# Kernel tuning notes

Measured on AMD Instinct MI355X. Metric: run time of the kernel, lower is better.

## Reference

```python
import jax, jax.numpy as jnp
import numpy as np

B, N, K = 64, 1024, 20
HEADS, DIM_K, DIM_V, CH_RAISE = 8, 32, 32, 64
C_CAT = 4 * 2 + DIM_V  # 44


def setup_inputs() -> dict:
    key = jax.random.key(0)
    ks = jax.random.split(key, 16)

    def w(k, shape):
        fan_in = shape[-1]
        return jax.random.normal(k, shape, dtype=jnp.float32) / np.sqrt(fan_in)

    def gamma(k, n):
        return 1.0 + 0.1 * jax.random.normal(k, (n,), dtype=jnp.float32)

    def beta(k, n):
        return 0.1 * jax.random.normal(k, (n,), dtype=jnp.float32)

    return {
        "x": jax.random.normal(ks[0], (B, N, 4), dtype=jnp.float32),
        "W_h": w(ks[1], (DIM_V, 4)),              # mlp_h: conv2d 4 -> dim_v, 1x1
        "W1": w(ks[2], (CH_RAISE, C_CAT)),        # mlp conv2d 44 -> 64
        "g1": gamma(ks[3], CH_RAISE), "b1": beta(ks[4], CH_RAISE),
        "W2": w(ks[5], (CH_RAISE, CH_RAISE)),     # mlp conv2d 64 -> 64
        "g2": gamma(ks[6], CH_RAISE), "b2": beta(ks[7], CH_RAISE),
        "W_v": w(ks[8], (DIM_V, C_CAT)),          # mlp_v conv1d 44 -> 32
        "gv": gamma(ks[9], DIM_V), "bv": beta(ks[10], DIM_V),
        "W_k": w(ks[11], (DIM_K, C_CAT)),         # mlp_k conv1d 44 -> 32
        "W_q": w(ks[12], (HEADS * DIM_K, CH_RAISE)),  # mlp_q conv1d 64 -> 256
        "gq": gamma(ks[13], HEADS * DIM_K), "bq": beta(ks[14], HEADS * DIM_K),
    }


def _forward(x, W_h, W1, g1, b1, W2, g2, b2, W_v, gv, bv, W_k, W_q, gq, bq):
    xyz = x[..., :4]                 # [B,N,4]
    feat = xyz                       # use_norm=False -> feature = xyz
    b, n, _ = xyz.shape

    # squared pairwise distances [B,N,N]
    sq = jnp.sum(xyz * xyz, axis=-1)
    dist = -2.0 * jnp.einsum('bnc,bmc->bnm', xyz, xyz) + sq[:, :, None] + sq[:, None, :]

    # KNN: K smallest distances
    _, knn_idx = jax.lax.top_k(-dist, K)          # [B,N,K]
    bidx = jnp.arange(b)[:, None, None]
    neighbor_xyz = xyz[bidx, knn_idx]             # [B,N,K,4]
    grouped = feat[bidx, knn_idx]                 # [B,N,K,4]

    feat_t = jnp.transpose(feat, (0, 2, 1))       # [B,4,N]
    grouped_c = jnp.transpose(grouped, (0, 3, 1, 2))          # [B,4,N,K]
    gnorm = grouped_c - feat_t[..., None]                     # [B,4,N,K]
    rel = jnp.transpose(neighbor_xyz - xyz[:, :, None, :], (0, 3, 1, 2))  # [B,4,N,K]

    pos = jnp.einsum('vc,bcnk->bvnk', W_h, rel)               # [B,32,N,K]
    center = jnp.broadcast_to(feat_t[..., None], (b, 4, n, K))
    feature = jnp.concatenate([gnorm, center, pos], axis=1)   # [B,44,N,K]

    # mlp: two 1x1 conv + BN(eval, affine) + ReLU
    h = jnp.einsum('oc,bcnk->bonk', W1, feature)
    h = jax.nn.relu(g1[None, :, None, None] * h + b1[None, :, None, None])
    h = jnp.einsum('oc,bcnk->bonk', W2, h)
    h = jax.nn.relu(g2[None, :, None, None] * h + b2[None, :, None, None])
    feature_q = jnp.max(h, axis=-1)                           # [B,64,N]

    q = jnp.einsum('oc,bcn->bon', W_q, feature_q)             # [B,256,N]
    q = jax.nn.relu(gq[None, :, None] * q + bq[None, :, None])
    q = q.reshape(b, HEADS, DIM_K, n)                         # [B,h,d,N]

    v = jnp.einsum('vc,bcnk->bvnk', W_v, feature)             # [B,32,N,K]
    v = gv[None, :, None, None] * v + bv[None, :, None, None]
    v = jnp.transpose(v, (0, 2, 1, 3))                        # [B,N,v,K]

    kk = jnp.einsum('dc,bcnk->bdnk', W_k, feature)            # [B,32,N,K]
    kk = jax.nn.softmax(kk, axis=-1)
    kk = jnp.transpose(kk, (0, 2, 1, 3))                      # [B,N,d,K]

    kv = jnp.einsum('bndk,bnvk->bdvn', kk, v)                 # [B,d,v,N]
    out = jnp.einsum('bhdn,bdvn->bhvn', q, kv)                # [B,h,v,N]
    out = out.reshape(b, HEADS * DIM_V, n)                    # [B,256,N]
    return xyz, out


def reference(x, W_h, W1, g1, b1, W2, g2, b2, W_v, gv, bv, W_k, W_q, gq, bq):
    return _forward(x, W_h, W1, g1, b1, W2, g2, b2, W_v, gv, bv, W_k, W_q, gq, bq)
```

## Files before the change

### kernel.cpp

```cpp
#include <hip/hip_runtime.h>
#include <math.h>

#define NPTS 1024
#define KNBR 20
#define CH 64


typedef __attribute__((ext_vector_type(8))) short s16x8;
typedef __attribute__((ext_vector_type(4))) float f32x4;

static __device__ __forceinline__ ushort f2bf(float f) {
  uint u = __float_as_uint(f);
  uint r = (u + 0x7FFFu + ((u >> 16) & 1u)) >> 16;
  return (ushort)r;
}

static __device__ __forceinline__ uint pkbf(float a, float b) {
  uint ua = __float_as_uint(a) + 0x8000u;
  uint ub = __float_as_uint(b) + 0x8000u;
  return __builtin_amdgcn_perm(ub, ua, 0x07060302);
}

static __device__ __forceinline__ int mbcnt64(unsigned long long m) {
  return __builtin_amdgcn_mbcnt_hi((uint)(m >> 32),
                                   __builtin_amdgcn_mbcnt_lo((uint)m, 0));
}

__global__ __launch_bounds__(256) void k_prep(
    const float* __restrict__ Wh, const float* __restrict__ W1,
    const float* __restrict__ g1, const float* __restrict__ b1,
    const float* __restrict__ Wv, const float* __restrict__ Wk,
    const float* __restrict__ W2, const float* __restrict__ Wq,
    float* __restrict__ wp, ushort* __restrict__ w2b,
    ushort* __restrict__ wqb, ushort* __restrict__ w1b) {
  int t = threadIdx.x;
  {
    int o = t >> 2, c = t & 3;
    float acc = W1[o * 40 + c];
    #pragma unroll
    for (int v = 0; v < 32; ++v) acc = fmaf(W1[o * 40 + 8 + v], Wh[v * 4 + c], acc);
    float g = g1[o];
    wp[t] = g * acc;
    wp[256 + t] = g * W1[o * 40 + 4 + c];
  }
  if (t < 128) {
    int d = t >> 2, c = t & 3;
    float av = Wv[d * 40 + c];
    float ak = Wk[d * 40 + c];
    #pragma unroll
    for (int u = 0; u < 32; ++u) {
      av = fmaf(Wv[d * 40 + 8 + u], Wh[u * 4 + c], av);
      ak = fmaf(Wk[d * 40 + 8 + u], Wh[u * 4 + c], ak);
    }
    wp[512 + t] = av;
    wp[640 + t] = Wv[d * 40 + 4 + c];
    wp[768 + t] = ak;
    wp[896 + t] = Wk[d * 40 + 4 + c];
  }
  #pragma unroll
  for (int i = 0; i < 16; ++i) w2b[t * 16 + i] = f2bf(W2[t * 16 + i]);
  for (int i = 0; i < 64; ++i) wqb[t * 64 + i] = f2bf(Wq[t * 64 + i]);
  __syncthreads();
  for (int idx = t; idx < 2048; idx += 256) {
    int ch = idx >> 5, kk = idx & 31;
    float v = 0.f;
    if (kk < 4) v = wp[ch * 4 + kk];
    else if (kk < 8) v = wp[256 + ch * 4 + (kk - 4)];
    else if (kk == 8) v = b1[ch];
    w1b[idx] = f2bf(v);
  }
}

__global__ __launch_bounds__(256) void k_knn(const float4* __restrict__ xv,
                                             ushort* __restrict__ knn,
                                             float4* __restrict__ outx) {
  __shared__ float4 sx[NPTS];
  __shared__ float ssq[NPTS];
  __shared__ uint s_sk[4][64];
  __shared__ ushort s_sj[4][64];

  int t = threadIdx.x;
  int b = blockIdx.x >> 5, grp = blockIdx.x & 31;
  for (int j = t; j < NPTS; j += 256) {
    float4 p = xv[b * NPTS + j];
    sx[j] = p;
    ssq[j] = p.x * p.x + p.y * p.y + p.z * p.z + p.w * p.w;
    if (grp == 0) outx[b * NPTS + j] = p;
  }
  __syncthreads();

  int w = t >> 6, l = t & 63;

  #pragma unroll 1
  for (int i = 0; i < 8; ++i) {
    int cloc = grp * 32 + w * 8 + i;
    int gid20 = (b * NPTS + cloc) * KNBR;
    float4 c = sx[cloc];
    uint u[16];
    uint mn = 0xFFFFFFFFu;
    #pragma unroll
    for (int s = 0; s < 16; ++s) {
      int j = s * 64 + l;
      float4 q = sx[j];
      float dot = c.x * q.x;
      dot = fmaf(c.y, q.y, dot);
      dot = fmaf(c.z, q.z, dot);
      dot = fmaf(c.w, q.w, dot);
      float key = fmaf(-2.f, dot, ssq[j]);
      uint uu = __float_as_uint(key);
      uu = ((int)uu < 0) ? ~uu : (uu | 0x80000000u);
      u[s] = uu;
      mn = min(mn, uu);
    }

    uint T0 = 0;
    #pragma unroll
    for (int bit = 31; bit >= 0; --bit) {
      uint cand = T0 | (1u << bit);
      if (__popcll(__ballot(mn < cand)) < 20) T0 = cand;
    }

    int scnt = 0;
    #pragma unroll
    for (int s = 0; s < 16; ++s) scnt += (int)__popcll(__ballot(u[s] <= T0));

    if (scnt <= 64) {
      int base = 0;
      #pragma unroll
      for (int s = 0; s < 16; ++s) {
        unsigned long long mask = __ballot(u[s] <= T0);
        if (u[s] <= T0) {
          int off = base + mbcnt64(mask);
          s_sk[w][off] = u[s];
          s_sj[w][off] = (ushort)(s * 64 + l);
        }
        base += (int)__popcll(mask);
      }
      asm volatile("s_waitcnt lgkmcnt(0)" ::: "memory");
      __builtin_amdgcn_sched_barrier(0);
      uint uk = (l < scnt) ? s_sk[w][l] : 0xFFFFFFFFu;
      uint uj = (l < scnt) ? (uint)s_sj[w][l] : 0xFFFFu;

      uint u20 = 0;
      #pragma unroll
      for (int bit = 31; bit >= 0; --bit) {
        uint cand = u20 | (1u << bit);
        if (__popcll(__ballot(uk < cand)) < 20) u20 = cand;
      }
      int m = (int)__popcll(__ballot(uk < u20));
      int r = 20 - m;
      uint jr = 0;
      #pragma unroll
      for (int bit = 10; bit >= 0; --bit) {
        uint cand = jr | (1u << bit);
        if (__popcll(__ballot((uk == u20) && (uj < cand))) < r) jr = cand;
      }
      bool sel = (uk < u20) || ((uk == u20) && (uj <= jr));
      unsigned long long smask = __ballot(sel);
      int off = mbcnt64(smask);
      if (sel) knn[gid20 + off] = (ushort)uj;
    } else {
      uint u20 = 0;
      #pragma unroll 1
      for (int bit = 31; bit >= 0; --bit) {
        uint cand = u20 | (1u << bit);
        int cnt = 0;
        #pragma unroll
        for (int s = 0; s < 16; ++s)
          cnt += (int)__popcll(__ballot(u[s] < cand));
        if (cnt < 20) u20 = cand;
      }
      int base = 0;
      #pragma unroll
      for (int s = 0; s < 16; ++s) {
        unsigned long long mask = __ballot(u[s] < u20);
        if (u[s] < u20) knn[gid20 + base + mbcnt64(mask)] = (ushort)(s * 64 + l);
        base += (int)__popcll(mask);
      }
      int r = 20 - base;
      #pragma unroll
      for (int s = 0; s < 16; ++s) {
        unsigned long long mask = __ballot(u[s] == u20);
        int pos = mbcnt64(mask);
        int cntm = (int)__popcll(mask);
        int take = (r < cntm) ? r : cntm;
        if ((u[s] == u20) && (pos < take))
          knn[gid20 + base + pos] = (ushort)(s * 64 + l);
        base += take;
        r -= take;
      }
    }
  }
}

__global__ __launch_bounds__(256) void k_fused(
    const float4* __restrict__ xv, const ushort* __restrict__ knn,
    const float* __restrict__ wp, const ushort* __restrict__ w1b,
    const ushort* __restrict__ w2b, const ushort* __restrict__ wqb,
    const float* __restrict__ g2, const float* __restrict__ b2,
    const float* __restrict__ gq, const float* __restrict__ bq,
    const float* __restrict__ gv, const float* __restrict__ bv,
    float* __restrict__ o1) {
  __shared__ __align__(16) char smem[51200];
  char* s_h1 = smem;
  ushort* s_qb = (ushort*)smem;
  ushort* s_eb = (ushort*)(smem + 10496);
  float* s_out = (float*)(smem + 10496);
  float4* s_rel = (float4*)(smem + 40960);
  char* s_fqb = smem + 46080;
  float4* s_ctr = (float4*)(smem + 48384);
  ushort* s_ab = (ushort*)(smem + 40960);

  int t = threadIdx.x;
  int gid0 = blockIdx.x * 16;
  int bbase = (gid0 >> 10) << 10;
  int b = gid0 >> 10;
  int n0 = gid0 & 1023;
  int w = t >> 6, l = t & 63;
  int g = l >> 4, lane16 = l & 15;

  if (t < 16) s_ctr[t] = xv[gid0 + t];
  #pragma unroll
  for (int it2 = 0; it2 < 2; ++it2) {
    int idx = t + it2 * 256;
    if (idx < 320) {
      int p = (int)(((uint)idx * 3277u) >> 16);
      int k = idx - p * 20;
      int nb = (int)knn[(size_t)(gid0 + p) * KNBR + k];
      float4 nx = xv[bbase + nb];
      float4 ct = xv[gid0 + p];
      s_rel[p * 20 + k] =
          make_float4(nx.x - ct.x, nx.y - ct.y, nx.z - ct.z, nx.w - ct.w);
    }
  }
  __syncthreads();

  {
    s16x8 ah[4];
    #pragma unroll
    for (int m = 0; m < 4; ++m)
      ah[m] = *(const s16x8*)(w1b + (m * 16 + lane16) * 32 + g * 8);
    s16x8 bz = {0, 0, 0, 0, 0, 0, 0, 0};
    s16x8 bone = bz;
    bone[0] = (short)0x3F80;
    #pragma unroll
    for (int q = 0; q < 5; ++q) {
      int col = w * 80 + q * 16 + lane16;
      s16x8 bf;
      if (g == 0) {
        float4 r = s_rel[lane16 * 20 + 5 * w + q];
        float4 ct = s_ctr[lane16];
        union { uint4 u; s16x8 s; } cv;
        cv.u.x = pkbf(r.x, r.y);
        cv.u.y = pkbf(r.z, r.w);
        cv.u.z = pkbf(ct.x, ct.y);
        cv.u.w = pkbf(ct.z, ct.w);
        bf = cv.s;
      } else {
        bf = (g == 1) ? bone : bz;
      }
      int swz = (col & 7) << 4;
      #pragma unroll
      for (int m = 0; m < 4; ++m) {
        f32x4 acc = {0.f, 0.f, 0.f, 0.f};
        acc = __builtin_amdgcn_mfma_f32_16x16x32_bf16(ah[m], bf, acc, 0, 0, 0);
        uint2 hv;
        hv.x = pkbf(fmaxf(acc[0], 0.f), fmaxf(acc[1], 0.f));
        hv.y = pkbf(fmaxf(acc[2], 0.f), fmaxf(acc[3], 0.f));
        int byteoff = col * 128 + (m * 16 + g * 4) * 2;
        *(uint2*)(s_h1 + (byteoff ^ swz)) = hv;
      }
    }
  }
  __syncthreads();

  {
    int row0 = w * 16 + g * 4;
    s16x8 af0 = *(const s16x8*)(w2b + (w * 16 + lane16) * 64 + g * 8);
    s16x8 af1 = *(const s16x8*)(w2b + (w * 16 + lane16) * 64 + 32 + g * 8);
    float4 g2v = *(const float4*)(g2 + row0);
    float4 b2v = *(const float4*)(b2 + row0);
    float mx0 = 0.f, mx1 = 0.f, mx2 = 0.f, mx3 = 0.f;
    #pragma unroll 4
    for (int kt = 0; kt < 20; ++kt) {
      int col = kt * 16 + lane16;
      int rowbyte = col * 128;
      int swz = (col & 7) << 4;
      s16x8 bf0 = *(const s16x8*)(s_h1 + ((rowbyte + g * 16) ^ swz));
      s16x8 bf1 = *(const s16x8*)(s_h1 + ((rowbyte + 64 + g * 16) ^ swz));
      f32x4 acc = {0.f, 0.f, 0.f, 0.f};
      acc = __builtin_amdgcn_mfma_f32_16x16x32_bf16(af0, bf0, acc, 0, 0, 0);
      acc = __builtin_amdgcn_mfma_f32_16x16x32_bf16(af1, bf1, acc, 0, 0, 0);
      mx0 = fmaxf(mx0, fmaxf(fmaf(g2v.x, acc[0], b2v.x), 0.f));
      mx1 = fmaxf(mx1, fmaxf(fmaf(g2v.y, acc[1], b2v.y), 0.f));
      mx2 = fmaxf(mx2, fmaxf(fmaf(g2v.z, acc[2], b2v.z), 0.f));
      mx3 = fmaxf(mx3, fmaxf(fmaf(g2v.w, acc[3], b2v.w), 0.f));
    }
    uint2 u2;
    u2.x = pkbf(mx0, mx1);
    u2.y = pkbf(mx2, mx3);
    *(uint2*)(s_fqb + lane16 * 144 + row0 * 2) = u2;
  }
  __syncthreads();

  {
    s16x8 af[4][2];
    #pragma unroll
    for (int mm = 0; mm < 4; ++mm) {
      int row = w * 64 + mm * 16 + lane16;
      af[mm][0] = *(const s16x8*)(wqb + row * 64 + g * 8);
      af[mm][1] = *(const s16x8*)(wqb + row * 64 + 32 + g * 8);
    }
    s16x8 bf0 = *(const s16x8*)(s_fqb + lane16 * 144 + 0 * 64 + g * 16);
    s16x8 bf1 = *(const s16x8*)(s_fqb + lane16 * 144 + 1 * 64 + g * 16);
    #pragma unroll
    for (int mm = 0; mm < 4; ++mm) {
      f32x4 acc = {0.f, 0.f, 0.f, 0.f};
      acc = __builtin_amdgcn_mfma_f32_16x16x32_bf16(af[mm][0], bf0, acc, 0, 0, 0);
      acc = __builtin_amdgcn_mfma_f32_16x16x32_bf16(af[mm][1], bf1, acc, 0, 0, 0);
      int rbase = w * 64 + mm * 16 + g * 4;
      int h = rbase >> 5, d0 = rbase & 31;
      float4 gqv = *(const float4*)(gq + rbase);
      float4 bqv = *(const float4*)(bq + rbase);
      float v0 = fmaxf(fmaf(gqv.x, acc[0], bqv.x), 0.f);
      float v1 = fmaxf(fmaf(gqv.y, acc[1], bqv.y), 0.f);
      float v2 = fmaxf(fmaf(gqv.z, acc[2], bqv.z), 0.f);
      float v3 = fmaxf(fmaf(gqv.w, acc[3], bqv.w), 0.f);
      uint2 u2;
      u2.x = pkbf(v0, v1);
      u2.y = pkbf(v2, v3);
      *(uint2*)(s_qb + lane16 * 328 + h * 40 + d0) = u2;
    }
  }

  uint vp[2][10];
  {
    int d = t & 31, phalf = t >> 5;
    float4 wr = *(const float4*)(wp + 512 + 256 + d * 4);
    float4 wc = *(const float4*)(wp + 512 + 384 + d * 4);
    float4 vr_ = *(const float4*)(wp + 512 + 0 + d * 4);
    float4 vc_ = *(const float4*)(wp + 512 + 128 + d * 4);
    float gvd = gv[d], bvd = bv[d];
    #pragma unroll
    for (int i = 0; i < 2; ++i) {
      int p = phalf + 8 * i;
      float4 ct = s_ctr[p];
      float cb = fmaf(wc.x, ct.x, fmaf(wc.y, ct.y, fmaf(wc.z, ct.z, wc.w * ct.w)));
      float ev[KNBR];
      float sum = 0.f;
      #pragma unroll
      for (int k = 0; k < KNBR; ++k) {
        float4 r = s_rel[p * 20 + k];
        float kkv =
            fmaf(wr.x, r.x, fmaf(wr.y, r.y, fmaf(wr.z, r.z, fmaf(wr.w, r.w, cb))));
        ev[k] = __expf(kkv);
        sum += ev[k];
      }
      float cbv = fmaf(vc_.x, ct.x, fmaf(vc_.y, ct.y, fmaf(vc_.z, ct.z, vc_.w * ct.w)));
      float vv[KNBR];
      #pragma unroll
      for (int k = 0; k < KNBR; ++k) {
        float4 r = s_rel[p * 20 + k];
        float raw =
            fmaf(vr_.x, r.x, fmaf(vr_.y, r.y, fmaf(vr_.z, r.z, fmaf(vr_.w, r.w, cbv))));
        vv[k] = fmaf(gvd, raw, bvd);
      }
      float rs = 1.0f / sum;
      #pragma unroll
      for (int k = 0; k < KNBR; ++k)
        s_eb[(p * 20 + k) * 40 + d] = f2bf(ev[k] * rs);
      #pragma unroll
      for (int k2 = 0; k2 < 10; ++k2) vp[i][k2] = pkbf(vv[k2 * 2], vv[k2 * 2 + 1]);
    }
  }
  __syncthreads();

  #pragma unroll
  for (int pi2 = 0; pi2 < 4; ++pi2) {
    int plo = pi2 & 1, ii = pi2 >> 1;
    int pi = 2 * w + plo + 8 * ii;
    s16x8 qa = *(const s16x8*)(s_qb + pi * 328 + (lane16 & 7) * 40 + g * 8);
    #pragma unroll
    for (int tile = 0; tile < 2; ++tile) {
      int k = tile * 16 + lane16;
      int kc = (k < KNBR) ? k : (KNBR - 1);
      s16x8 eb = *(const s16x8*)(s_eb + (pi * 20 + kc) * 40 + g * 8);
      f32x4 acc = {0.f, 0.f, 0.f, 0.f};
      acc = __builtin_amdgcn_mfma_f32_16x16x32_bf16(qa, eb, acc, 0, 0, 0);
      if (g < 2) {
        if (k < KNBR) {
          #pragma unroll
          for (int r = 0; r < 4; ++r)
            s_ab[pi * 320 + (g * 4 + r) * 40 + k] = f2bf(acc[r]);
        } else {
          #pragma unroll
          for (int r = 0; r < 4; ++r) s_ab[pi * 320 + (g * 4 + r) * 40 + k] = 0;
        }
      }
    }
  }
  __syncthreads();

  #pragma unroll
  for (int pi2 = 0; pi2 < 4; ++pi2) {
    int plo = pi2 & 1, ii = pi2 >> 1;
    int pi = 2 * w + plo + 8 * ii;
    s16x8 aa = *(const s16x8*)(s_ab + pi * 320 + (lane16 & 7) * 40 + g * 8);
    #pragma unroll
    for (int vt = 0; vt < 2; ++vt) {
      int srcl4 = ((plo * 32 + vt * 16 + lane16) << 2);
      uint bu[4];
      #pragma unroll
      for (int i = 0; i < 4; ++i) {
        uint t0 = (uint)__builtin_amdgcn_ds_bpermute(srcl4, (int)vp[ii][i]);
        uint t1 = (uint)__builtin_amdgcn_ds_bpermute(srcl4, (int)vp[ii][4 + i]);
        uint t2 = (i < 2)
                      ? (uint)__builtin_amdgcn_ds_bpermute(srcl4, (int)vp[ii][8 + i])
                      : 0u;
        bu[i] = (g == 0) ? t0 : (g == 1) ? t1 : (g == 2) ? t2 : 0u;
      }
      union { uint4 u; s16x8 s; } bb;
      bb.u.x = bu[0]; bb.u.y = bu[1]; bb.u.z = bu[2]; bb.u.w = bu[3];
      f32x4 acc = {0.f, 0.f, 0.f, 0.f};
      acc = __builtin_amdgcn_mfma_f32_16x16x32_bf16(aa, bb.s, acc, 0, 0, 0);
      if (g < 2) {
        int v = vt * 16 + lane16;
        #pragma unroll
        for (int r = 0; r < 4; ++r) {
          int h = g * 4 + r;
          s_out[(h * 32 + v) * 17 + pi] = acc[r];
        }
      }
    }
  }
  __syncthreads();

  #pragma unroll
  for (int e = 0; e < 16; ++e) {
    int idx = t + e * 256;
    int hv = idx >> 4, pp = idx & 15;
    o1[b * 262144 + hv * 1024 + n0 + pp] = s_out[hv * 17 + pp];
  }
}

extern "C" void kernel_launch(void* const* d_in, const int* in_sizes, int n_in,
                              void* d_out, int out_size, void* d_ws, size_t ws_size,
                              hipStream_t stream) {
  const float* x = (const float*)d_in[0];
  const float* Wh = (const float*)d_in[1];
  const float* W1 = (const float*)d_in[2];
  const float* g1 = (const float*)d_in[3];
  const float* b1 = (const float*)d_in[4];
  const float* W2 = (const float*)d_in[5];
  const float* g2 = (const float*)d_in[6];
  const float* b2 = (const float*)d_in[7];
  const float* Wv = (const float*)d_in[8];
  const float* gv = (const float*)d_in[9];
  const float* bv = (const float*)d_in[10];
  const float* Wk = (const float*)d_in[11];
  const float* Wq = (const float*)d_in[12];
  const float* gq = (const float*)d_in[13];
  const float* bq = (const float*)d_in[14];
  float* out = (float*)d_out;

  ushort* knn = (ushort*)d_ws;
  float* wp = (float*)((char*)d_ws + 19398656);
  ushort* w2b = (ushort*)((char*)d_ws + 19402752);
  ushort* wqb = (ushort*)((char*)d_ws + 19410944);
  ushort* w1b = (ushort*)((char*)d_ws + 19443712);

  hipLaunchKernelGGL(k_prep, dim3(1), dim3(256), 0, stream, Wh, W1, g1, b1, Wv, Wk,
                     W2, Wq, wp, w2b, wqb, w1b);
  hipLaunchKernelGGL(k_knn, dim3(2048), dim3(256), 0, stream, (const float4*)x, knn,
                     (float4*)out);
  hipLaunchKernelGGL(k_fused, dim3(4096), dim3(256), 0, stream, (const float4*)x,
                     knn, wp, w1b, w2b, wqb, g2, b2, gq, bq, gv, bv, out + 262144);
}
```

Baseline: 169.2 us.

## Halve points per block in KNN and fused kernels to raise occupancy

The KNN kernel now processes 16 query points per block instead of 32, doubling its grid. The fused attention kernel handles 8 points per block instead of 16, halving shared memory so more blocks can be resident. To keep the MFMA tiles full, it remaps columns to (k, point) pairs and merges the two halves with a cross-lane shuffle max. The cost is that each KNN block restages all 1024 points for half the work, and half the lanes are idle in the q-projection MFMA epilogue.

```diff
diff --git a/kernel.cpp b/kernel.cpp
--- a/kernel.cpp
+++ b/kernel.cpp
@@ -80,7 +80,7 @@
   __shared__ ushort s_sj[4][64];
 
   int t = threadIdx.x;
-  int b = blockIdx.x >> 5, grp = blockIdx.x & 31;
+  int b = blockIdx.x >> 6, grp = blockIdx.x & 63;
   for (int j = t; j < NPTS; j += 256) {
     float4 p = xv[b * NPTS + j];
     sx[j] = p;
@@ -92,8 +92,8 @@
   int w = t >> 6, l = t & 63;
 
   #pragma unroll 1
-  for (int i = 0; i < 8; ++i) {
-    int cloc = grp * 32 + w * 8 + i;
+  for (int i = 0; i < 4; ++i) {
+    int cloc = grp * 16 + w * 4 + i;
     int gid20 = (b * NPTS + cloc) * KNBR;
     float4 c = sx[cloc];
     uint u[16];
@@ -201,37 +201,33 @@
     const float* __restrict__ gq, const float* __restrict__ bq,
     const float* __restrict__ gv, const float* __restrict__ bv,
     float* __restrict__ o1) {
-  __shared__ __align__(16) char smem[51200];
+  __shared__ __align__(16) char smem[25600];
   char* s_h1 = smem;
   ushort* s_qb = (ushort*)smem;
-  ushort* s_eb = (ushort*)(smem + 10496);
-  float* s_out = (float*)(smem + 10496);
-  float4* s_rel = (float4*)(smem + 40960);
-  char* s_fqb = smem + 46080;
-  float4* s_ctr = (float4*)(smem + 48384);
-  ushort* s_ab = (ushort*)(smem + 40960);
+  ushort* s_eb = (ushort*)(smem + 5248);
+  float* s_out = (float*)(smem + 5248);
+  float4* s_rel = (float4*)(smem + 20480);
+  char* s_fqb = smem + 23040;
+  float4* s_ctr = (float4*)(smem + 24192);
+  ushort* s_ab = (ushort*)(smem + 20480);
 
   int t = threadIdx.x;
-  int gid0 = blockIdx.x * 16;
+  int gid0 = blockIdx.x * 8;
   int bbase = (gid0 >> 10) << 10;
   int b = gid0 >> 10;
   int n0 = gid0 & 1023;
   int w = t >> 6, l = t & 63;
   int g = l >> 4, lane16 = l & 15;
 
-  if (t < 16) s_ctr[t] = xv[gid0 + t];
-  #pragma unroll
-  for (int it2 = 0; it2 < 2; ++it2) {
-    int idx = t + it2 * 256;
-    if (idx < 320) {
-      int p = (int)(((uint)idx * 3277u) >> 16);
-      int k = idx - p * 20;
-      int nb = (int)knn[(size_t)(gid0 + p) * KNBR + k];
-      float4 nx = xv[bbase + nb];
-      float4 ct = xv[gid0 + p];
-      s_rel[p * 20 + k] =
-          make_float4(nx.x - ct.x, nx.y - ct.y, nx.z - ct.z, nx.w - ct.w);
-    }
+  if (t < 8) s_ctr[t] = xv[gid0 + t];
+  if (t < 160) {
+    int p = (int)(((uint)t * 3277u) >> 16);
+    int k = t - p * 20;
+    int nb = (int)knn[(size_t)(gid0 + p) * KNBR + k];
+    float4 nx = xv[bbase + nb];
+    float4 ct = xv[gid0 + p];
+    s_rel[p * 20 + k] =
+        make_float4(nx.x - ct.x, nx.y - ct.y, nx.z - ct.z, nx.w - ct.w);
   }
   __syncthreads();
 
@@ -243,13 +239,14 @@
     s16x8 bz = {0, 0, 0, 0, 0, 0, 0, 0};
     s16x8 bone = bz;
     bone[0] = (short)0x3F80;
-    #pragma unroll
-    for (int q = 0; q < 5; ++q) {
-      int col = w * 80 + q * 16 + lane16;
+    #pragma unroll 1
+    for (int q = w; q < 10; q += 4) {
+      int col = q * 16 + lane16;
+      int kk = col >> 3, p = col & 7;
       s16x8 bf;
       if (g == 0) {
-        float4 r = s_rel[lane16 * 20 + 5 * w + q];
-        float4 ct = s_ctr[lane16];
+        float4 r = s_rel[p * 20 + kk];
+        float4 ct = s_ctr[p];
         union { uint4 u; s16x8 s; } cv;
         cv.u.x = pkbf(r.x, r.y);
         cv.u.y = pkbf(r.z, r.w);
@@ -281,8 +278,8 @@
     float4 g2v = *(const float4*)(g2 + row0);
     float4 b2v = *(const float4*)(b2 + row0);
     float mx0 = 0.f, mx1 = 0.f, mx2 = 0.f, mx3 = 0.f;
-    #pragma unroll 4
-    for (int kt = 0; kt < 20; ++kt) {
+    #pragma unroll 2
+    for (int kt = 0; kt < 10; ++kt) {
       int col = kt * 16 + lane16;
       int rowbyte = col * 128;
       int swz = (col & 7) << 4;
@@ -296,10 +293,16 @@
       mx2 = fmaxf(mx2, fmaxf(fmaf(g2v.z, acc[2], b2v.z), 0.f));
       mx3 = fmaxf(mx3, fmaxf(fmaf(g2v.w, acc[3], b2v.w), 0.f));
     }
-    uint2 u2;
-    u2.x = pkbf(mx0, mx1);
-    u2.y = pkbf(mx2, mx3);
-    *(uint2*)(s_fqb + lane16 * 144 + row0 * 2) = u2;
+    mx0 = fmaxf(mx0, __shfl_xor(mx0, 8));
+    mx1 = fmaxf(mx1, __shfl_xor(mx1, 8));
+    mx2 = fmaxf(mx2, __shfl_xor(mx2, 8));
+    mx3 = fmaxf(mx3, __shfl_xor(mx3, 8));
+    if ((lane16 & 8) == 0) {
+      uint2 u2;
+      u2.x = pkbf(mx0, mx1);
+      u2.y = pkbf(mx2, mx3);
+      *(uint2*)(s_fqb + lane16 * 144 + row0 * 2) = u2;
+    }
   }
   __syncthreads();
 
@@ -311,74 +314,71 @@
       af[mm][0] = *(const s16x8*)(wqb + row * 64 + g * 8);
       af[mm][1] = *(const s16x8*)(wqb + row * 64 + 32 + g * 8);
     }
-    s16x8 bf0 = *(const s16x8*)(s_fqb + lane16 * 144 + 0 * 64 + g * 16);
-    s16x8 bf1 = *(const s16x8*)(s_fqb + lane16 * 144 + 1 * 64 + g * 16);
+    int p8 = lane16 & 7;
+    s16x8 bf0 = *(const s16x8*)(s_fqb + p8 * 144 + g * 16);
+    s16x8 bf1 = *(const s16x8*)(s_fqb + p8 * 144 + 64 + g * 16);
+    bool active = (lane16 < 8);
     #pragma unroll
     for (int mm = 0; mm < 4; ++mm) {
       f32x4 acc = {0.f, 0.f, 0.f, 0.f};
       acc = __builtin_amdgcn_mfma_f32_16x16x32_bf16(af[mm][0], bf0, acc, 0, 0, 0);
       acc = __builtin_amdgcn_mfma_f32_16x16x32_bf16(af[mm][1], bf1, acc, 0, 0, 0);
-      int rbase = w * 64 + mm * 16 + g * 4;
-      int h = rbase >> 5, d0 = rbase & 31;
-      float4 gqv = *(const float4*)(gq + rbase);
-      float4 bqv = *(const float4*)(bq + rbase);
-      float v0 = fmaxf(fmaf(gqv.x, acc[0], bqv.x), 0.f);
-      float v1 = fmaxf(fmaf(gqv.y, acc[1], bqv.y), 0.f);
-      float v2 = fmaxf(fmaf(gqv.z, acc[2], bqv.z), 0.f);
-      float v3 = fmaxf(fmaf(gqv.w, acc[3], bqv.w), 0.f);
-      uint2 u2;
-      u2.x = pkbf(v0, v1);
-      u2.y = pkbf(v2, v3);
-      *(uint2*)(s_qb + lane16 * 328 + h * 40 + d0) = u2;
-    }
-  }
-
-  uint vp[2][10];
+      if (active) {
+        int rbase = w * 64 + mm * 16 + g * 4;
+        int h = rbase >> 5, d0 = rbase & 31;
+        float4 gqv = *(const float4*)(gq + rbase);
+        float4 bqv = *(const float4*)(bq + rbase);
+        float v0 = fmaxf(fmaf(gqv.x, acc[0], bqv.x), 0.f);
+        float v1 = fmaxf(fmaf(gqv.y, acc[1], bqv.y), 0.f);
+        float v2 = fmaxf(fmaf(gqv.z, acc[2], bqv.z), 0.f);
+        float v3 = fmaxf(fmaf(gqv.w, acc[3], bqv.w), 0.f);
+        uint2 u2;
+        u2.x = pkbf(v0, v1);
+        u2.y = pkbf(v2, v3);
+        *(uint2*)(s_qb + lane16 * 328 + h * 40 + d0) = u2;
+      }
+    }
+  }
+
+  uint vp[10];
   {
-    int d = t & 31, phalf = t >> 5;
+    int d = t & 31, p = t >> 5;
     float4 wr = *(const float4*)(wp + 512 + 256 + d * 4);
     float4 wc = *(const float4*)(wp + 512 + 384 + d * 4);
     float4 vr_ = *(const float4*)(wp + 512 + 0 + d * 4);
     float4 vc_ = *(const float4*)(wp + 512 + 128 + d * 4);
     float gvd = gv[d], bvd = bv[d];
-    #pragma unroll
-    for (int i = 0; i < 2; ++i) {
-      int p = phalf + 8 * i;
-      float4 ct = s_ctr[p];
-      float cb = fmaf(wc.x, ct.x, fmaf(wc.y, ct.y, fmaf(wc.z, ct.z, wc.w * ct.w)));
-      float ev[KNBR];
-      float sum = 0.f;
-      #pragma unroll
-      for (int k = 0; k < KNBR; ++k) {
-        float4 r = s_rel[p * 20 + k];
-        float kkv =
-            fmaf(wr.x, r.x, fmaf(wr.y, r.y, fmaf(wr.z, r.z, fmaf(wr.w, r.w, cb))));
-        ev[k] = __expf(kkv);
-        sum += ev[k];
-      }
-      float cbv = fmaf(vc_.x, ct.x, fmaf(vc_.y, ct.y, fmaf(vc_.z, ct.z, vc_.w * ct.w)));
-      float vv[KNBR];
-      #pragma unroll
-      for (int k = 0; k < KNBR; ++k) {
-        float4 r = s_rel[p * 20 + k];
-        float raw =
-            fmaf(vr_.x, r.x, fmaf(vr_.y, r.y, fmaf(vr_.z, r.z, fmaf(vr_.w, r.w, cbv))));
-        vv[k] = fmaf(gvd, raw, bvd);
-      }
-      float rs = 1.0f / sum;
-      #pragma unroll
-      for (int k = 0; k < KNBR; ++k)
-        s_eb[(p * 20 + k) * 40 + d] = f2bf(ev[k] * rs);
-      #pragma unroll
-      for (int k2 = 0; k2 < 10; ++k2) vp[i][k2] = pkbf(vv[k2 * 2], vv[k2 * 2 + 1]);
-    }
+    float4 ct = s_ctr[p];
+    float cb = fmaf(wc.x, ct.x, fmaf(wc.y, ct.y, fmaf(wc.z, ct.z, wc.w * ct.w)));
+    float ev[KNBR];
+    float sum = 0.f;
+    #pragma unroll
+    for (int k = 0; k < KNBR; ++k) {
+      float4 r = s_rel[p * 20 + k];
+      float kkv = fmaf(wr.x, r.x, fmaf(wr.y, r.y, fmaf(wr.z, r.z, fmaf(wr.w, r.w, cb))));
+      ev[k] = __expf(kkv);
+      sum += ev[k];
+    }
+    float cbv = fmaf(vc_.x, ct.x, fmaf(vc_.y, ct.y, fmaf(vc_.z, ct.z, vc_.w * ct.w)));
+    float vv[KNBR];
+    #pragma unroll
+    for (int k = 0; k < KNBR; ++k) {
+      float4 r = s_rel[p * 20 + k];
+      float raw = fmaf(vr_.x, r.x, fmaf(vr_.y, r.y, fmaf(vr_.z, r.z, fmaf(vr_.w, r.w, cbv))));
+      vv[k] = fmaf(gvd, raw, bvd);
+    }
+    float rs = 1.0f / sum;
+    #pragma unroll
+    for (int k = 0; k < KNBR; ++k)
+      s_eb[(p * 20 + k) * 40 + d] = f2bf(ev[k] * rs);
+    #pragma unroll
+    for (int k2 = 0; k2 < 10; ++k2) vp[k2] = pkbf(vv[k2 * 2], vv[k2 * 2 + 1]);
   }
   __syncthreads();
 
   #pragma unroll
-  for (int pi2 = 0; pi2 < 4; ++pi2) {
-    int plo = pi2 & 1, ii = pi2 >> 1;
-    int pi = 2 * w + plo + 8 * ii;
+  for (int pi2 = 0; pi2 < 2; ++pi2) {
+    int pi = 2 * w + pi2;
     s16x8 qa = *(const s16x8*)(s_qb + pi * 328 + (lane16 & 7) * 40 + g * 8);
     #pragma unroll
     for (int tile = 0; tile < 2; ++tile) {
@@ -402,20 +402,19 @@
   __syncthreads();
 
   #pragma unroll
-  for (int pi2 = 0; pi2 < 4; ++pi2) {
-    int plo = pi2 & 1, ii = pi2 >> 1;
-    int pi = 2 * w + plo + 8 * ii;
+  for (int pi2 = 0; pi2 < 2; ++pi2) {
+    int pi = 2 * w + pi2;
     s16x8 aa = *(const s16x8*)(s_ab + pi * 320 + (lane16 & 7) * 40 + g * 8);
     #pragma unroll
     for (int vt = 0; vt < 2; ++vt) {
-      int srcl4 = ((plo * 32 + vt * 16 + lane16) << 2);
+      int srcl4 = ((pi2 * 32 + vt * 16 + lane16) << 2);
       uint bu[4];
       #pragma unroll
       for (int i = 0; i < 4; ++i) {
-        uint t0 = (uint)__builtin_amdgcn_ds_bpermute(srcl4, (int)vp[ii][i]);
-        uint t1 = (uint)__builtin_amdgcn_ds_bpermute(srcl4, (int)vp[ii][4 + i]);
+        uint t0 = (uint)__builtin_amdgcn_ds_bpermute(srcl4, (int)vp[i]);
+        uint t1 = (uint)__builtin_amdgcn_ds_bpermute(srcl4, (int)vp[4 + i]);
         uint t2 = (i < 2)
-                      ? (uint)__builtin_amdgcn_ds_bpermute(srcl4, (int)vp[ii][8 + i])
+                      ? (uint)__builtin_amdgcn_ds_bpermute(srcl4, (int)vp[8 + i])
                       : 0u;
         bu[i] = (g == 0) ? t0 : (g == 1) ? t1 : (g == 2) ? t2 : 0u;
       }
@@ -428,7 +427,7 @@
         #pragma unroll
         for (int r = 0; r < 4; ++r) {
           int h = g * 4 + r;
-          s_out[(h * 32 + v) * 17 + pi] = acc[r];
+          s_out[(h * 32 + v) * 9 + pi] = acc[r];
         }
       }
     }
@@ -436,10 +435,10 @@
   __syncthreads();
 
   #pragma unroll
-  for (int e = 0; e < 16; ++e) {
+  for (int e = 0; e < 8; ++e) {
     int idx = t + e * 256;
-    int hv = idx >> 4, pp = idx & 15;
-    o1[b * 262144 + hv * 1024 + n0 + pp] = s_out[hv * 17 + pp];
+    int hv = idx >> 3, pp = idx & 7;
+    o1[b * 262144 + hv * 1024 + n0 + pp] = s_out[hv * 9 + pp];
   }
 }
 
@@ -471,8 +470,8 @@
 
   hipLaunchKernelGGL(k_prep, dim3(1), dim3(256), 0, stream, Wh, W1, g1, b1, Wv, Wk,
                      W2, Wq, wp, w2b, wqb, w1b);
-  hipLaunchKernelGGL(k_knn, dim3(2048), dim3(256), 0, stream, (const float4*)x, knn,
+  hipLaunchKernelGGL(k_knn, dim3(4096), dim3(256), 0, stream, (const float4*)x, knn,
                      (float4*)out);
-  hipLaunchKernelGGL(k_fused, dim3(4096), dim3(256), 0, stream, (const float4*)x,
+  hipLaunchKernelGGL(k_fused, dim3(8192), dim3(256), 0, stream, (const float4*)x,
                      knn, wp, w1b, w2b, wqb, g2, b2, gq, bq, gv, bv, out + 262144);
 }
```

After: 176.0 us. 1.04x slower.
